# Kernel optimization log

Hardware: AMD Instinct MI355X
Metric: run time of the kernel (lower is better)

Reference implementation:

```python
import jax, jax.numpy as jnp
import numpy as np

N = 100000      # nodes
E = 1600000     # edges (avg degree 16)
IN = 128        # in_channels
H = 128         # hidden_channels
EPS = 1e-5      # BatchNorm eps


def setup_inputs() -> dict:
    key = jax.random.key(0)
    ks = jax.random.split(key, 10)
    x = jax.random.normal(ks[0], (N, IN), jnp.float32)
    edge_index = jax.random.randint(ks[1], (2, E), 0, N, dtype=jnp.int32)

    def lin(k, i, o):
        return jax.random.normal(k, (i, o), jnp.float32) * (1.0 / np.sqrt(i))

    d2 = 2 * H
    return {
        "x": x, "edge_index": edge_index,
        # SAGEConv 1: 128 -> 128
        "w1l": lin(ks[2], IN, H), "w1r": lin(ks[3], IN, H), "b1": jnp.zeros((H,), jnp.float32),
        "g1": jnp.ones((H,), jnp.float32), "be1": jnp.zeros((H,), jnp.float32),
        "m1": jnp.zeros((H,), jnp.float32), "v1": jnp.ones((H,), jnp.float32),
        # SAGEConv 2: 128 -> 256
        "w2l": lin(ks[4], H, d2), "w2r": lin(ks[5], H, d2), "b2": jnp.zeros((d2,), jnp.float32),
        "g2": jnp.ones((d2,), jnp.float32), "be2": jnp.zeros((d2,), jnp.float32),
        "m2": jnp.zeros((d2,), jnp.float32), "v2": jnp.ones((d2,), jnp.float32),
        # SAGEConv 3: 256 -> 256
        "w3l": lin(ks[6], d2, d2), "w3r": lin(ks[7], d2, d2), "b3": jnp.zeros((d2,), jnp.float32),
        "g3": jnp.ones((d2,), jnp.float32), "be3": jnp.zeros((d2,), jnp.float32),
        "m3": jnp.zeros((d2,), jnp.float32), "v3": jnp.ones((d2,), jnp.float32),
    }


def _sage_conv(x, src, dst, wl, wr, b):
    # PyG SAGEConv (mean aggr): out = mean_{j in N(i)} x_j @ W_l + x_i @ W_r + b
    agg = jax.ops.segment_sum(x[src], dst, num_segments=N)          # [N, d_in]
    deg = jax.ops.segment_sum(jnp.ones((src.shape[0],), x.dtype), dst, num_segments=N)
    mean = agg / jnp.maximum(deg, 1.0)[:, None]
    return mean @ wl + x @ wr + b


def _bn(x, g, b, m, v):
    # BatchNorm1d in eval mode (running stats); dropout is a no-op in eval
    return (x - m) * jax.lax.rsqrt(v + EPS) * g + b


def reference(x, edge_index,
              w1l, w1r, b1, g1, be1, m1, v1,
              w2l, w2r, b2, g2, be2, m2, v2,
              w3l, w3r, b3, g3, be3, m3, v3):
    src, dst = edge_index[0], edge_index[1]
    h = _bn(jax.nn.relu(_sage_conv(x, src, dst, w1l, w1r, b1)), g1, be1, m1, v1)
    h = _bn(jax.nn.relu(_sage_conv(h, src, dst, w2l, w2r, b2)), g2, be2, m2, v2)
    h = _bn(jax.nn.relu(_sage_conv(h, src, dst, w3l, w3r, b3)), g3, be3, m3, v3)
    return h  # [N, 2*H]
```

## Files before the change

### kernel.cpp

```cpp
#include <hip/hip_runtime.h>

#define NNODES 100000
#define NEDGES 1600000
#define EPSV 1e-5f

#define NB   391
#define BCAP 4608
#define EPB  4096

typedef __attribute__((ext_vector_type(8))) short bf16x8;
typedef __attribute__((ext_vector_type(4))) float f32x4;

#if defined(__has_builtin)
#  if __has_builtin(__builtin_amdgcn_cvt_pk_f32_fp8) && __has_builtin(__builtin_amdgcn_cvt_pk_fp8_f32)
#    define HAS_FP8_CVT 1
#  endif
#endif
#ifndef HAS_FP8_CVT
#  define HAS_FP8_CVT 0
#endif

__device__ __forceinline__ ushort f2bf(float f) {
    union { float f; uint u; } c; c.f = f;
    uint u = c.u;
    return (ushort)((u + 0x7fffu + ((u >> 16) & 1u)) >> 16);
}
__device__ __forceinline__ uint pack2(float f0, float f1) {
    return (uint)f2bf(f0) | ((uint)f2bf(f1) << 16);
}

#if !HAS_FP8_CVT
__device__ __forceinline__ float fp8_dec1(uint b) {
    uint e = (b >> 3) & 0xFu, m = b & 7u, s = b >> 7;
    union { uint u; float f; } c;
    c.u = e ? ((s << 31) | ((e + 120u) << 23) | (m << 20)) : (s << 31);
    return c.f;
}
__device__ __forceinline__ uint fp8_enc1(float x) {
    union { float f; uint u; } c; c.f = x;
    uint u = c.u, s = u >> 31;
    float ax = fabsf(x);
    if (ax < 0.015625f) return s << 7;
    if (ax > 448.0f)    return (s << 7) | 0x7Eu;
    u = u + 0x7FFFFu + ((u >> 20) & 1u);
    uint e = ((u >> 23) & 0xFFu) - 120u;
    uint m = (u >> 20) & 7u;
    if (e > 15u) return (s << 7) | 0x7Eu;
    return (s << 7) | (e << 3) | m;
}
#endif

__device__ __forceinline__ void accf8(float* a, uint2 v) {
#if HAS_FP8_CVT
    auto p0 = __builtin_amdgcn_cvt_pk_f32_fp8((int)v.x, false);
    auto p1 = __builtin_amdgcn_cvt_pk_f32_fp8((int)v.x, true);
    auto p2 = __builtin_amdgcn_cvt_pk_f32_fp8((int)v.y, false);
    auto p3 = __builtin_amdgcn_cvt_pk_f32_fp8((int)v.y, true);
    a[0] += p0[0]; a[1] += p0[1]; a[2] += p1[0]; a[3] += p1[1];
    a[4] += p2[0]; a[5] += p2[1]; a[6] += p3[0]; a[7] += p3[1];
#else
    a[0] += fp8_dec1(v.x & 0xFFu);         a[1] += fp8_dec1((v.x >> 8) & 0xFFu);
    a[2] += fp8_dec1((v.x >> 16) & 0xFFu); a[3] += fp8_dec1(v.x >> 24);
    a[4] += fp8_dec1(v.y & 0xFFu);         a[5] += fp8_dec1((v.y >> 8) & 0xFFu);
    a[6] += fp8_dec1((v.y >> 16) & 0xFFu); a[7] += fp8_dec1(v.y >> 24);
#endif
}

__device__ __forceinline__ uint f2fp8(float f) {
#if HAS_FP8_CVT
    return ((uint)__builtin_amdgcn_cvt_pk_fp8_f32(f, f, 0, false)) & 0xFFu;
#else
    return fp8_enc1(f);
#endif
}

__device__ __forceinline__ uint packf8_4(float f0, float f1, float f2, float f3) {
#if HAS_FP8_CVT
    int r = 0;
    r = __builtin_amdgcn_cvt_pk_fp8_f32(f0, f1, r, false);
    r = __builtin_amdgcn_cvt_pk_fp8_f32(f2, f3, r, true);
    return (uint)r;
#else
    return fp8_enc1(f0) | (fp8_enc1(f1) << 8) | (fp8_enc1(f2) << 16) | (fp8_enc1(f3) << 24);
#endif
}

__global__ __launch_bounds__(256) void part_kernel(
    const int* __restrict__ src, const int* __restrict__ dst,
    int* __restrict__ cursor, uint2* __restrict__ pairs, int E)
{
    __shared__ int lcnt[NB];
    __shared__ int lbase[NB];
    const int t = threadIdx.x;
    for (int i = t; i < NB; i += 256) lcnt[i] = 0;
    __syncthreads();

    const int base = blockIdx.x * EPB;
    const int lim  = min(base + EPB, E);

    for (int e = base + t; e < lim; e += 256)
        atomicAdd(&lcnt[((unsigned)dst[e]) >> 8], 1);
    __syncthreads();

    for (int i = t; i < NB; i += 256) {
        int c = lcnt[i];
        lbase[i] = c ? atomicAdd(&cursor[i], c) : 0;
        lcnt[i] = 0;
    }
    __syncthreads();

    for (int e = base + t; e < lim; e += 256) {
        int d = dst[e];
        int b = ((unsigned)d) >> 8;
        int p = lbase[b] + atomicAdd(&lcnt[b], 1);
        if (p < BCAP) pairs[(size_t)b * BCAP + p] = make_uint2((uint)src[e], (uint)d);
    }
}

__global__ __launch_bounds__(512) void bscan_kernel(const int* __restrict__ cursor,
                                                    int* __restrict__ colBase)
{
    __shared__ int s[512];
    int t = threadIdx.x;
    int v = (t < NB) ? min(cursor[t], BCAP) : 0;
    s[t] = v;
    __syncthreads();
    #pragma unroll
    for (int off = 1; off < 512; off <<= 1) {
        int a = (t >= off) ? s[t - off] : 0;
        __syncthreads();
        s[t] += a;
        __syncthreads();
    }
    if (t < NB) colBase[t] = s[t] - v;
}

__global__ __launch_bounds__(256) void csr_fin_kernel(
    const uint2* __restrict__ pairs, const int* __restrict__ cursor,
    const int* __restrict__ colBase, int* __restrict__ cnt,
    int* __restrict__ rptr, int* __restrict__ col, int n)
{
    __shared__ int lcnt[256];
    __shared__ int lofs[256];
    const int b = blockIdx.x;
    const int t = threadIdx.x;
    const int ecnt  = min(cursor[b], BCAP);
    const int cbase = colBase[b];
    const uint2* __restrict__ pp = pairs + (size_t)b * BCAP;

    lcnt[t] = 0;
    __syncthreads();
    for (int e = t; e < ecnt; e += 256)
        atomicAdd(&lcnt[pp[e].y & 255u], 1);
    __syncthreads();

    const int v = lcnt[t];
    lofs[t] = v;
    __syncthreads();
    #pragma unroll
    for (int off = 1; off < 256; off <<= 1) {
        int a = (t >= off) ? lofs[t - off] : 0;
        __syncthreads();
        lofs[t] += a;
        __syncthreads();
    }
    const int excl = lofs[t] - v;

    const int node = (b << 8) + t;
    if (node < n) {
        cnt[node]  = v;
        rptr[node] = cbase + excl + v;
    }
    __syncthreads();
    lcnt[t] = excl;
    __syncthreads();

    for (int e = t; e < ecnt; e += 256) {
        uint2 pr = pp[e];
        int p = cbase + atomicAdd(&lcnt[pr.y & 255u], 1);
        col[p] = (int)pr.x;
    }
}

__global__ void cvt_x_kernel(const float* __restrict__ in, ushort* __restrict__ outb,
                             unsigned char* __restrict__ out8, int n4) {
    int i = blockIdx.x * blockDim.x + threadIdx.x;
    if (i < n4) {
        float4 v = ((const float4*)in)[i];
        ushort4 o;
        o.x = f2bf(v.x); o.y = f2bf(v.y); o.z = f2bf(v.z); o.w = f2bf(v.w);
        ((ushort4*)outb)[i] = o;
        ((uint*)out8)[i] = packf8_4(v.x, v.y, v.z, v.w);
    }
}

__global__ void wT_all_kernel(
    const float* __restrict__ w1l, const float* __restrict__ w1r,
    const float* __restrict__ w2l, const float* __restrict__ w2r,
    const float* __restrict__ w3l, const float* __restrict__ w3r,
    ushort* __restrict__ t1l, ushort* __restrict__ t1r,
    ushort* __restrict__ t2l, ushort* __restrict__ t2r,
    ushort* __restrict__ t3l, ushort* __restrict__ t3r)
{
    int idx = blockIdx.x * blockDim.x + threadIdx.x;
    const float* w; ushort* wt; int K, Nout, i;
    if      (idx <  16384) { w = w1l; wt = t1l; K = 128; Nout = 128; i = idx; }
    else if (idx <  32768) { w = w1r; wt = t1r; K = 128; Nout = 128; i = idx - 16384; }
    else if (idx <  65536) { w = w2l; wt = t2l; K = 128; Nout = 256; i = idx - 32768; }
    else if (idx <  98304) { w = w2r; wt = t2r; K = 128; Nout = 256; i = idx - 65536; }
    else if (idx < 163840) { w = w3l; wt = t3l; K = 256; Nout = 256; i = idx - 98304; }
    else if (idx < 229376) { w = w3r; wt = t3r; K = 256; Nout = 256; i = idx - 163840; }
    else return;
    int k = i / Nout, n = i - k * Nout;
    wt[(size_t)n * K + k] = f2bf(w[i]);
}

template<int D>
__global__ __launch_bounds__(256) void gather_f8(
    const unsigned char* __restrict__ x, const int* __restrict__ rptr,
    const int* __restrict__ cnt, const int* __restrict__ col,
    ushort* __restrict__ agg, int n)
{
    constexpr int TPN = D / 8;
    constexpr int NPB = 256 / TPN;
    const int node = blockIdx.x * NPB + threadIdx.x / TPN;
    const int lane = threadIdx.x % TPN;
    if (node >= n) return;

    const int c   = cnt[node];
    const int end = rptr[node];
    const uint2* __restrict__ xp = (const uint2*)x + lane;

    float a[8] = {};
    int e = end - c;
    for (; e + 7 < end; e += 8) {
        int s0 = col[e],     s1 = col[e + 1], s2 = col[e + 2], s3 = col[e + 3];
        int s4 = col[e + 4], s5 = col[e + 5], s6 = col[e + 6], s7 = col[e + 7];
        uint2 v0 = xp[(size_t)s0 * TPN];
        uint2 v1 = xp[(size_t)s1 * TPN];
        uint2 v2 = xp[(size_t)s2 * TPN];
        uint2 v3 = xp[(size_t)s3 * TPN];
        uint2 v4 = xp[(size_t)s4 * TPN];
        uint2 v5 = xp[(size_t)s5 * TPN];
        uint2 v6 = xp[(size_t)s6 * TPN];
        uint2 v7 = xp[(size_t)s7 * TPN];
        accf8(a, v0); accf8(a, v1); accf8(a, v2); accf8(a, v3);
        accf8(a, v4); accf8(a, v5); accf8(a, v6); accf8(a, v7);
    }
    for (; e + 1 < end; e += 2) {
        uint2 v0 = xp[(size_t)col[e] * TPN];
        uint2 v1 = xp[(size_t)col[e + 1] * TPN];
        accf8(a, v0); accf8(a, v1);
    }
    if (e < end) accf8(a, xp[(size_t)col[e] * TPN]);

    const float inv = 1.0f / fmaxf((float)c, 1.0f);
    uint4 o;
    o.x = pack2(a[0] * inv, a[1] * inv);
    o.y = pack2(a[2] * inv, a[3] * inv);
    o.z = pack2(a[4] * inv, a[5] * inv);
    o.w = pack2(a[6] * inv, a[7] * inv);
    ((uint4*)agg)[(size_t)node * TPN + lane] = o;
}

template<int DIN, int DOUT, bool OUTF32, bool WRITE8>
__global__ __launch_bounds__(256) void mfma_layer(
    const ushort* __restrict__ xin, const ushort* __restrict__ agg,
    const ushort* __restrict__ wlT, const ushort* __restrict__ wrT,
    const float* __restrict__ bias, const float* __restrict__ gamma,
    const float* __restrict__ beta, const float* __restrict__ rmean,
    const float* __restrict__ rvar, void* __restrict__ outp,
    unsigned char* __restrict__ out8, int M)
{
    constexpr int BM = 128, BN = 128, BK = 32;
    constexpr int LDA = BK + 8;
    __shared__ ushort As[BM * LDA];
    __shared__ ushort Bs[BN * LDA];

    const int tid  = threadIdx.x;
    const int lane = tid & 63;
    const int wid  = tid >> 6;
    const int wm   = (wid & 1) * 64;
    const int wn   = (wid >> 1) * 64;
    const int lr   = lane & 15;
    const int quad = lane >> 4;

    const int row0 = blockIdx.x * BM;
    const int col0 = blockIdx.y * BN;

    f32x4 acc[4][4] = {};

    const int s_row  = tid >> 2;
    const int s_koff = (tid & 3) * 8;

    #pragma unroll
    for (int phase = 0; phase < 2; ++phase) {
        const ushort* __restrict__ A = phase ? xin : agg;
        const ushort* __restrict__ W = phase ? wrT : wlT;

        for (int k0 = 0; k0 < DIN; k0 += BK) {
            int gr0 = row0 + s_row;       gr0 = gr0 < M ? gr0 : M - 1;
            int gr1 = row0 + s_row + 64;  gr1 = gr1 < M ? gr1 : M - 1;
            uint4 a0v = *(const uint4*)(A + (size_t)gr0 * DIN + k0 + s_koff);
            uint4 a1v = *(const uint4*)(A + (size_t)gr1 * DIN + k0 + s_koff);
            uint4 b0v = *(const uint4*)(W + (size_t)(col0 + s_row) * DIN + k0 + s_koff);
            uint4 b1v = *(const uint4*)(W + (size_t)(col0 + s_row + 64) * DIN + k0 + s_koff);

            __syncthreads();
            *(uint4*)&As[s_row * LDA + s_koff]        = a0v;
            *(uint4*)&As[(s_row + 64) * LDA + s_koff] = a1v;
            *(uint4*)&Bs[s_row * LDA + s_koff]        = b0v;
            *(uint4*)&Bs[(s_row + 64) * LDA + s_koff] = b1v;
            __syncthreads();

            bf16x8 af[4], bf[4];
            #pragma unroll
            for (int t = 0; t < 4; ++t) {
                af[t] = *(const bf16x8*)&As[(wm + t * 16 + lr) * LDA + quad * 8];
                bf[t] = *(const bf16x8*)&Bs[(wn + t * 16 + lr) * LDA + quad * 8];
            }
            #pragma unroll
            for (int mt = 0; mt < 4; ++mt)
                #pragma unroll
                for (int nt = 0; nt < 4; ++nt)
                    acc[mt][nt] = __builtin_amdgcn_mfma_f32_16x16x32_bf16(
                        af[mt], bf[nt], acc[mt][nt], 0, 0, 0);
        }
    }

    float bj[4], sj[4], mj[4], bej[4];
    #pragma unroll
    for (int nt = 0; nt < 4; ++nt) {
        int gc = col0 + wn + nt * 16 + lr;
        bj[nt]  = bias[gc];
        sj[nt]  = rsqrtf(rvar[gc] + EPSV) * gamma[gc];
        mj[nt]  = rmean[gc];
        bej[nt] = beta[gc];
    }
    #pragma unroll
    for (int mt = 0; mt < 4; ++mt) {
        #pragma unroll
        for (int r = 0; r < 4; ++r) {
            int grow = row0 + wm + mt * 16 + quad * 4 + r;
            if (grow < M) {
                #pragma unroll
                for (int nt = 0; nt < 4; ++nt) {
                    int gc = col0 + wn + nt * 16 + lr;
                    float h = acc[mt][nt][r] + bj[nt];
                    h = fmaxf(h, 0.0f);
                    h = (h - mj[nt]) * sj[nt] + bej[nt];
                    if (OUTF32) ((float*)outp)[(size_t)grow * DOUT + gc] = h;
                    else        ((ushort*)outp)[(size_t)grow * DOUT + gc] = f2bf(h);
                    if (WRITE8) out8[(size_t)grow * DOUT + gc] = (unsigned char)f2fp8(h);
                }
            }
        }
    }
}

extern "C" void kernel_launch(void* const* d_in, const int* in_sizes, int n_in,
                              void* d_out, int out_size, void* d_ws, size_t ws_size,
                              hipStream_t stream) {
    const int N = NNODES;
    const int E = NEDGES;

    const float* x   = (const float*)d_in[0];
    const int*   ei  = (const int*)d_in[1];
    const int*   src = ei;
    const int*   dst = ei + E;

    const float* w1l = (const float*)d_in[2];
    const float* w1r = (const float*)d_in[3];
    const float* b1  = (const float*)d_in[4];
    const float* g1  = (const float*)d_in[5];
    const float* be1 = (const float*)d_in[6];
    const float* m1  = (const float*)d_in[7];
    const float* v1  = (const float*)d_in[8];

    const float* w2l = (const float*)d_in[9];
    const float* w2r = (const float*)d_in[10];
    const float* b2  = (const float*)d_in[11];
    const float* g2  = (const float*)d_in[12];
    const float* be2 = (const float*)d_in[13];
    const float* m2  = (const float*)d_in[14];
    const float* v2  = (const float*)d_in[15];

    const float* w3l = (const float*)d_in[16];
    const float* w3r = (const float*)d_in[17];
    const float* b3  = (const float*)d_in[18];
    const float* g3  = (const float*)d_in[19];
    const float* be3 = (const float*)d_in[20];
    const float* m3  = (const float*)d_in[21];
    const float* v3  = (const float*)d_in[22];

    float* out = (float*)d_out;

    char*   wp      = (char*)d_ws;
    int*    cnt     = (int*)wp;     wp += (size_t)N * sizeof(int);
    int*    rptr    = (int*)wp;     wp += (size_t)N * sizeof(int);
    int*    cursor  = (int*)wp;     wp += 512 * sizeof(int);
    int*    colBase = (int*)wp;     wp += 512 * sizeof(int);
    int*    col     = (int*)wp;     wp += (size_t)E * sizeof(int);
    uint2*  pairs   = (uint2*)wp;   wp += (size_t)NB * BCAP * sizeof(uint2);
    ushort* xbf     = (ushort*)wp;  wp += (size_t)N * 128 * sizeof(ushort);
    ushort* h1      = (ushort*)wp;  wp += (size_t)N * 128 * sizeof(ushort);
    ushort* h2      = (ushort*)wp;  wp += (size_t)N * 256 * sizeof(ushort);
    ushort* aggb    = (ushort*)wp;  wp += (size_t)N * 256 * sizeof(ushort);
    unsigned char* h2f8 = (unsigned char*)wp; wp += (size_t)N * 256;
    ushort* w1lT    = (ushort*)wp;  wp += 128 * 128 * sizeof(ushort);
    ushort* w1rT    = (ushort*)wp;  wp += 128 * 128 * sizeof(ushort);
    ushort* w2lT    = (ushort*)wp;  wp += 256 * 128 * sizeof(ushort);
    ushort* w2rT    = (ushort*)wp;  wp += 256 * 128 * sizeof(ushort);
    ushort* w3lT    = (ushort*)wp;  wp += 256 * 256 * sizeof(ushort);
    ushort* w3rT    = (ushort*)wp;

    unsigned char* xf8  = (unsigned char*)pairs;
    unsigned char* h1f8 = (unsigned char*)pairs;

    const int T = 256;

    hipMemsetAsync(cursor, 0, 512 * sizeof(int), stream);
    part_kernel<<<(E + EPB - 1) / EPB, 256, 0, stream>>>(src, dst, cursor, pairs, E);
    bscan_kernel<<<1, 512, 0, stream>>>(cursor, colBase);
    csr_fin_kernel<<<NB, 256, 0, stream>>>(pairs, cursor, colBase, cnt, rptr, col, N);

    cvt_x_kernel<<<((N * 128 / 4) + T - 1) / T, T, 0, stream>>>(x, xbf, xf8, N * 128 / 4);
    wT_all_kernel<<<229376 / 256, 256, 0, stream>>>(w1l, w1r, w2l, w2r, w3l, w3r,
                                                    w1lT, w1rT, w2lT, w2rT, w3lT, w3rT);

    const dim3 g1g((N + 127) / 128, 1);
    const dim3 g2g((N + 127) / 128, 2);

    gather_f8<128><<<(N + 15) / 16, 256, 0, stream>>>(xf8, rptr, cnt, col, aggb, N);
    mfma_layer<128, 128, false, true><<<g1g, 256, 0, stream>>>(
        xbf, aggb, w1lT, w1rT, b1, g1, be1, m1, v1, h1, h1f8, N);

    gather_f8<128><<<(N + 15) / 16, 256, 0, stream>>>(h1f8, rptr, cnt, col, aggb, N);
    mfma_layer<128, 256, false, true><<<g2g, 256, 0, stream>>>(
        h1, aggb, w2lT, w2rT, b2, g2, be2, m2, v2, h2, h2f8, N);

    gather_f8<256><<<(N + 7) / 8, 256, 0, stream>>>(h2f8, rptr, cnt, col, aggb, N);
    mfma_layer<256, 256, true, false><<<g2g, 256, 0, stream>>>(
        h2, aggb, w3lT, w3rT, b3, g3, be3, m3, v3, out, nullptr, N);
}
```

Measured before the change: 494.5 us.

## Use direct global-to-LDS loads with swizzle, widen gather loads, merge setup kernels

The GEMM tile staging now uses global_load_lds to copy 16-byte chunks straight into LDS, with an XOR-swizzled unpadded layout, so the register round-trip is gone. The fp8 neighbour gather now has each thread load 16 bytes per edge instead of 8, halving the threads per node. The x conversion and weight transpose kernels are merged into one launch. Risks include LDS bank conflicts if the swizzle does not match the MFMA read pattern, and the gather having less memory-level parallelism with a 4-deep unroll.

```diff
diff --git a/kernel.cpp b/kernel.cpp
--- a/kernel.cpp
+++ b/kernel.cpp
@@ -19,6 +19,11 @@
 #ifndef HAS_FP8_CVT
 #  define HAS_FP8_CVT 0
 #endif
+
+#define GLD16(gp, lp)                                                          \
+    __builtin_amdgcn_global_load_lds(                                          \
+        (const __attribute__((address_space(1))) void*)(gp),                   \
+        (__attribute__((address_space(3))) void*)(lp), 16, 0, 0)
 
 __device__ __forceinline__ ushort f2bf(float f) {
     union { float f; uint u; } c; c.f = f;
@@ -65,6 +70,10 @@
     a[6] += fp8_dec1((v.y >> 16) & 0xFFu); a[7] += fp8_dec1(v.y >> 24);
 #endif
 }
+__device__ __forceinline__ void accf8x16(float* a, uint4 v) {
+    accf8(a,     make_uint2(v.x, v.y));
+    accf8(a + 8, make_uint2(v.z, v.w));
+}
 
 __device__ __forceinline__ uint f2fp8(float f) {
 #if HAS_FP8_CVT
@@ -73,7 +82,6 @@
     return fp8_enc1(f);
 #endif
 }
-
 __device__ __forceinline__ uint packf8_4(float f0, float f1, float f2, float f3) {
 #if HAS_FP8_CVT
     int r = 0;
@@ -182,19 +190,9 @@
     }
 }
 
-__global__ void cvt_x_kernel(const float* __restrict__ in, ushort* __restrict__ outb,
-                             unsigned char* __restrict__ out8, int n4) {
-    int i = blockIdx.x * blockDim.x + threadIdx.x;
-    if (i < n4) {
-        float4 v = ((const float4*)in)[i];
-        ushort4 o;
-        o.x = f2bf(v.x); o.y = f2bf(v.y); o.z = f2bf(v.z); o.w = f2bf(v.w);
-        ((ushort4*)outb)[i] = o;
-        ((uint*)out8)[i] = packf8_4(v.x, v.y, v.z, v.w);
-    }
-}
-
-__global__ void wT_all_kernel(
+__global__ void setup_kernel(
+    const float* __restrict__ x, ushort* __restrict__ xbf,
+    unsigned char* __restrict__ xf8, int n4,
     const float* __restrict__ w1l, const float* __restrict__ w1r,
     const float* __restrict__ w2l, const float* __restrict__ w2r,
     const float* __restrict__ w3l, const float* __restrict__ w3r,
@@ -203,13 +201,22 @@
     ushort* __restrict__ t3l, ushort* __restrict__ t3r)
 {
     int idx = blockIdx.x * blockDim.x + threadIdx.x;
-    const float* w; ushort* wt; int K, Nout, i;
-    if      (idx <  16384) { w = w1l; wt = t1l; K = 128; Nout = 128; i = idx; }
-    else if (idx <  32768) { w = w1r; wt = t1r; K = 128; Nout = 128; i = idx - 16384; }
-    else if (idx <  65536) { w = w2l; wt = t2l; K = 128; Nout = 256; i = idx - 32768; }
-    else if (idx <  98304) { w = w2r; wt = t2r; K = 128; Nout = 256; i = idx - 65536; }
-    else if (idx < 163840) { w = w3l; wt = t3l; K = 256; Nout = 256; i = idx - 98304; }
-    else if (idx < 229376) { w = w3r; wt = t3r; K = 256; Nout = 256; i = idx - 163840; }
+    if (idx < n4) {
+        float4 v = ((const float4*)x)[idx];
+        ushort4 o;
+        o.x = f2bf(v.x); o.y = f2bf(v.y); o.z = f2bf(v.z); o.w = f2bf(v.w);
+        ((ushort4*)xbf)[idx] = o;
+        ((uint*)xf8)[idx] = packf8_4(v.x, v.y, v.z, v.w);
+        return;
+    }
+    int i = idx - n4;
+    const float* w; ushort* wt; int K, Nout;
+    if      (i <  16384) { w = w1l; wt = t1l; K = 128; Nout = 128; }
+    else if (i <  32768) { w = w1r; wt = t1r; K = 128; Nout = 128; i -= 16384; }
+    else if (i <  65536) { w = w2l; wt = t2l; K = 128; Nout = 256; i -= 32768; }
+    else if (i <  98304) { w = w2r; wt = t2r; K = 128; Nout = 256; i -= 65536; }
+    else if (i < 163840) { w = w3l; wt = t3l; K = 256; Nout = 256; i -= 98304; }
+    else if (i < 229376) { w = w3r; wt = t3r; K = 256; Nout = 256; i -= 163840; }
     else return;
     int k = i / Nout, n = i - k * Nout;
     wt[(size_t)n * K + k] = f2bf(w[i]);
@@ -221,7 +228,7 @@
     const int* __restrict__ cnt, const int* __restrict__ col,
     ushort* __restrict__ agg, int n)
 {
-    constexpr int TPN = D / 8;
+    constexpr int TPN = D / 16;
     constexpr int NPB = 256 / TPN;
     const int node = blockIdx.x * NPB + threadIdx.x / TPN;
     const int lane = threadIdx.x % TPN;
@@ -229,38 +236,33 @@
 
     const int c   = cnt[node];
     const int end = rptr[node];
-    const uint2* __restrict__ xp = (const uint2*)x + lane;
-
-    float a[8] = {};
+    const uint4* __restrict__ xp = (const uint4*)x + lane;
+
+    float a[16] = {};
     int e = end - c;
-    for (; e + 7 < end; e += 8) {
-        int s0 = col[e],     s1 = col[e + 1], s2 = col[e + 2], s3 = col[e + 3];
-        int s4 = col[e + 4], s5 = col[e + 5], s6 = col[e + 6], s7 = col[e + 7];
-        uint2 v0 = xp[(size_t)s0 * TPN];
-        uint2 v1 = xp[(size_t)s1 * TPN];
-        uint2 v2 = xp[(size_t)s2 * TPN];
-        uint2 v3 = xp[(size_t)s3 * TPN];
-        uint2 v4 = xp[(size_t)s4 * TPN];
-        uint2 v5 = xp[(size_t)s5 * TPN];
-        uint2 v6 = xp[(size_t)s6 * TPN];
-        uint2 v7 = xp[(size_t)s7 * TPN];
-        accf8(a, v0); accf8(a, v1); accf8(a, v2); accf8(a, v3);
-        accf8(a, v4); accf8(a, v5); accf8(a, v6); accf8(a, v7);
-    }
-    for (; e + 1 < end; e += 2) {
-        uint2 v0 = xp[(size_t)col[e] * TPN];
-        uint2 v1 = xp[(size_t)col[e + 1] * TPN];
-        accf8(a, v0); accf8(a, v1);
-    }
-    if (e < end) accf8(a, xp[(size_t)col[e] * TPN]);
+    for (; e + 3 < end; e += 4) {
+        int s0 = col[e], s1 = col[e + 1], s2 = col[e + 2], s3 = col[e + 3];
+        uint4 v0 = xp[(size_t)s0 * TPN];
+        uint4 v1 = xp[(size_t)s1 * TPN];
+        uint4 v2 = xp[(size_t)s2 * TPN];
+        uint4 v3 = xp[(size_t)s3 * TPN];
+        accf8x16(a, v0); accf8x16(a, v1); accf8x16(a, v2); accf8x16(a, v3);
+    }
+    for (; e < end; ++e) accf8x16(a, xp[(size_t)col[e] * TPN]);
 
     const float inv = 1.0f / fmaxf((float)c, 1.0f);
-    uint4 o;
-    o.x = pack2(a[0] * inv, a[1] * inv);
-    o.y = pack2(a[2] * inv, a[3] * inv);
-    o.z = pack2(a[4] * inv, a[5] * inv);
-    o.w = pack2(a[6] * inv, a[7] * inv);
-    ((uint4*)agg)[(size_t)node * TPN + lane] = o;
+    uint4 o0, o1;
+    o0.x = pack2(a[0] * inv,  a[1] * inv);
+    o0.y = pack2(a[2] * inv,  a[3] * inv);
+    o0.z = pack2(a[4] * inv,  a[5] * inv);
+    o0.w = pack2(a[6] * inv,  a[7] * inv);
+    o1.x = pack2(a[8] * inv,  a[9] * inv);
+    o1.y = pack2(a[10] * inv, a[11] * inv);
+    o1.z = pack2(a[12] * inv, a[13] * inv);
+    o1.w = pack2(a[14] * inv, a[15] * inv);
+    uint4* op = (uint4*)agg + (size_t)node * (2 * TPN) + lane * 2;
+    op[0] = o0;
+    op[1] = o1;
 }
 
 template<int DIN, int DOUT, bool OUTF32, bool WRITE8>
@@ -273,9 +275,8 @@
     unsigned char* __restrict__ out8, int M)
 {
     constexpr int BM = 128, BN = 128, BK = 32;
-    constexpr int LDA = BK + 8;
-    __shared__ ushort As[BM * LDA];
-    __shared__ ushort Bs[BN * LDA];
+    __shared__ ushort As[BM * BK];
+    __shared__ ushort Bs[BN * BK];
 
     const int tid  = threadIdx.x;
     const int lane = tid & 63;
@@ -290,34 +291,49 @@
 
     f32x4 acc[4][4] = {};
 
-    const int s_row  = tid >> 2;
-    const int s_koff = (tid & 3) * 8;
+    const int sr  = (wid << 5) + (lane >> 2);
+    const int sc  = (lane & 3) ^ ((sr >> 1) & 3);
+    const int grA0 = min(row0 + sr,      M - 1);
+    const int grA1 = min(row0 + sr + 16, M - 1);
+    const int grB0 = col0 + sr;
+    const int grB1 = col0 + sr + 16;
+    ushort* ldsA0 = As + wid * 1024;
+    ushort* ldsA1 = As + wid * 1024 + 512;
+    ushort* ldsB0 = Bs + wid * 1024;
+    ushort* ldsB1 = Bs + wid * 1024 + 512;
+
+    int aoff[4], boff[4];
+    #pragma unroll
+    for (int t = 0; t < 4; ++t) {
+        int ra = wm + t * 16 + lr;
+        aoff[t] = (ra * 4 + (quad ^ ((ra >> 1) & 3))) * 8;
+        int rb = wn + t * 16 + lr;
+        boff[t] = (rb * 4 + (quad ^ ((rb >> 1) & 3))) * 8;
+    }
 
     #pragma unroll
     for (int phase = 0; phase < 2; ++phase) {
         const ushort* __restrict__ A = phase ? xin : agg;
         const ushort* __restrict__ W = phase ? wrT : wlT;
 
+        const ushort* pa0 = A + (size_t)grA0 * DIN + sc * 8;
+        const ushort* pa1 = A + (size_t)grA1 * DIN + sc * 8;
+        const ushort* pb0 = W + (size_t)grB0 * DIN + sc * 8;
+        const ushort* pb1 = W + (size_t)grB1 * DIN + sc * 8;
+
         for (int k0 = 0; k0 < DIN; k0 += BK) {
-            int gr0 = row0 + s_row;       gr0 = gr0 < M ? gr0 : M - 1;
-            int gr1 = row0 + s_row + 64;  gr1 = gr1 < M ? gr1 : M - 1;
-            uint4 a0v = *(const uint4*)(A + (size_t)gr0 * DIN + k0 + s_koff);
-            uint4 a1v = *(const uint4*)(A + (size_t)gr1 * DIN + k0 + s_koff);
-            uint4 b0v = *(const uint4*)(W + (size_t)(col0 + s_row) * DIN + k0 + s_koff);
-            uint4 b1v = *(const uint4*)(W + (size_t)(col0 + s_row + 64) * DIN + k0 + s_koff);
-
             __syncthreads();
-            *(uint4*)&As[s_row * LDA + s_koff]        = a0v;
-            *(uint4*)&As[(s_row + 64) * LDA + s_koff] = a1v;
-            *(uint4*)&Bs[s_row * LDA + s_koff]        = b0v;
-            *(uint4*)&Bs[(s_row + 64) * LDA + s_koff] = b1v;
+            GLD16(pa0 + k0, ldsA0);
+            GLD16(pa1 + k0, ldsA1);
+            GLD16(pb0 + k0, ldsB0);
+            GLD16(pb1 + k0, ldsB1);
             __syncthreads();
 
             bf16x8 af[4], bf[4];
             #pragma unroll
             for (int t = 0; t < 4; ++t) {
-                af[t] = *(const bf16x8*)&As[(wm + t * 16 + lr) * LDA + quad * 8];
-                bf[t] = *(const bf16x8*)&Bs[(wn + t * 16 + lr) * LDA + quad * 8];
+                af[t] = *(const bf16x8*)&As[aoff[t]];
+                bf[t] = *(const bf16x8*)&Bs[boff[t]];
             }
             #pragma unroll
             for (int mt = 0; mt < 4; ++mt)
@@ -417,29 +433,28 @@
     unsigned char* xf8  = (unsigned char*)pairs;
     unsigned char* h1f8 = (unsigned char*)pairs;
 
-    const int T = 256;
-
     hipMemsetAsync(cursor, 0, 512 * sizeof(int), stream);
     part_kernel<<<(E + EPB - 1) / EPB, 256, 0, stream>>>(src, dst, cursor, pairs, E);
     bscan_kernel<<<1, 512, 0, stream>>>(cursor, colBase);
     csr_fin_kernel<<<NB, 256, 0, stream>>>(pairs, cursor, colBase, cnt, rptr, col, N);
 
-    cvt_x_kernel<<<((N * 128 / 4) + T - 1) / T, T, 0, stream>>>(x, xbf, xf8, N * 128 / 4);
-    wT_all_kernel<<<229376 / 256, 256, 0, stream>>>(w1l, w1r, w2l, w2r, w3l, w3r,
-                                                    w1lT, w1rT, w2lT, w2rT, w3lT, w3rT);
+    const int n4 = N * 128 / 4;
+    setup_kernel<<<(n4 + 229376) / 256, 256, 0, stream>>>(
+        x, xbf, xf8, n4, w1l, w1r, w2l, w2r, w3l, w3r,
+        w1lT, w1rT, w2lT, w2rT, w3lT, w3rT);
 
     const dim3 g1g((N + 127) / 128, 1);
     const dim3 g2g((N + 127) / 128, 2);
 
-    gather_f8<128><<<(N + 15) / 16, 256, 0, stream>>>(xf8, rptr, cnt, col, aggb, N);
+    gather_f8<128><<<(N + 31) / 32, 256, 0, stream>>>(xf8, rptr, cnt, col, aggb, N);
     mfma_layer<128, 128, false, true><<<g1g, 256, 0, stream>>>(
         xbf, aggb, w1lT, w1rT, b1, g1, be1, m1, v1, h1, h1f8, N);
 
-    gather_f8<128><<<(N + 15) / 16, 256, 0, stream>>>(h1f8, rptr, cnt, col, aggb, N);
+    gather_f8<128><<<(N + 31) / 32, 256, 0, stream>>>(h1f8, rptr, cnt, col, aggb, N);
     mfma_layer<128, 256, false, true><<<g2g, 256, 0, stream>>>(
         h1, aggb, w2lT, w2rT, b2, g2, be2, m2, v2, h2, h2f8, N);
 
-    gather_f8<256><<<(N + 7) / 8, 256, 0, stream>>>(h2f8, rptr, cnt, col, aggb, N);
+    gather_f8<256><<<(N + 15) / 16, 256, 0, stream>>>(h2f8, rptr, cnt, col, aggb, N);
     mfma_layer<256, 256, true, false><<<g2g, 256, 0, stream>>>(
         h2, aggb, w3lT, w3rT, b3, g3, be3, m3, v3, out, nullptr, N);
 }
```

Result: no change. 501.4 us (+1.4%).
